# Kernel optimization log

Measured on AMD Instinct MI355X. Metric: run time of the kernel, lower is better.

Reference implementation:

```python
import jax, jax.numpy as jnp
import numpy as np

A_CUBIC = -0.5  # Keys cubic-convolution parameter (order-3 spline approximation)


def _cubic(t):
    # Keys cubic interpolation kernel, support (-2, 2)
    at = jnp.abs(t)
    at2 = at * at
    at3 = at2 * at
    a = A_CUBIC
    w_inner = (a + 2.0) * at3 - (a + 3.0) * at2 + 1.0          # |t| <= 1
    w_outer = a * at3 - 5.0 * a * at2 + 8.0 * a * at - 4.0 * a  # 1 < |t| < 2
    return jnp.where(at <= 1.0, w_inner, jnp.where(at < 2.0, w_outer, 0.0))


def _spline_upsample_matrix(n_out, n_ctrl):
    # (n_out, n_ctrl) dense weight matrix interpolating control points to the
    # full-resolution axis with the cubic kernel; edge taps clamped (nearest).
    u = jnp.arange(n_out, dtype=jnp.float32) * (n_ctrl - 1) / (n_out - 1)
    i0 = jnp.floor(u).astype(jnp.int32)
    taps = i0[:, None] + jnp.arange(-1, 3)                      # (n_out, 4)
    w = _cubic(u[:, None] - taps.astype(jnp.float32))           # (n_out, 4)
    taps_c = jnp.clip(taps, 0, n_ctrl - 1)
    B = jnp.zeros((n_out, n_ctrl), jnp.float32)
    B = B.at[jnp.arange(n_out)[:, None], taps_c].add(w)
    return B


def _elastic_warp(img, displacement):
    # img: (H, W, C); displacement: (2, 3, 3) control-point displacements (dy, dx)
    H, W, C = img.shape
    By = _spline_upsample_matrix(H, displacement.shape[1])      # (H, 3)
    Bx = _spline_upsample_matrix(W, displacement.shape[2])      # (W, 3)
    disp = jnp.einsum('hy,dyx,wx->dhw', By, displacement, Bx)   # (2, H, W)

    yy = jnp.arange(H, dtype=jnp.float32)[:, None] + disp[0]    # sample coords
    xx = jnp.arange(W, dtype=jnp.float32)[None, :] + disp[1]
    iy0 = jnp.floor(yy).astype(jnp.int32)
    ix0 = jnp.floor(xx).astype(jnp.int32)

    out = jnp.zeros_like(img)
    # 4x4 cubic tap stencil (fixed small loop; each iteration is one full gather)
    for a in range(-1, 3):
        ty = iy0 + a
        wy = _cubic(yy - ty.astype(jnp.float32))                # (H, W)
        tyc = jnp.clip(ty, 0, H - 1)
        for b in range(-1, 3):
            tx = ix0 + b
            wx = _cubic(xx - tx.astype(jnp.float32))            # (H, W)
            txc = jnp.clip(tx, 0, W - 1)
            out = out + (wy * wx)[..., None] * img[tyc, txc]    # gather (H,W,C)
    return out


def setup_inputs() -> dict:
    key = jax.random.key(0)
    k1, k2 = jax.random.split(key)
    H, W, C = 2048, 4096, 3
    inputs = jax.random.normal(k1, (H, W, C), dtype=jnp.float32)
    displacement = jax.random.normal(k2, (2, 3, 3), dtype=jnp.float32)
    return {"inputs": inputs, "displacement": displacement}


def reference(inputs, displacement):
    # module draws displacement ~ N(0,1)*5 internally; externalized here
    return _elastic_warp(inputs, displacement * 5.0)
```

## Files before the change

kernel.cpp:

```cpp
#include <hip/hip_runtime.h>
#include <math.h>

constexpr int H = 2048;
constexpr int W = 4096;
constexpr int RS = W * 3;

__device__ __forceinline__ float k_inner(float t) {
    return fmaf(fmaf(1.5f, t, -2.5f), t * t, 1.0f);
}
__device__ __forceinline__ float k_outer(float t) {
    return fmaf(fmaf(fmaf(-0.5f, t, 2.5f), t, -4.0f), t, 2.0f);
}
__device__ __forceinline__ float cubic_w(float t) {
    float at = fabsf(t);
    if (at <= 1.0f) return k_inner(at);
    if (at < 2.0f)  return k_outer(at);
    return 0.0f;
}

__global__ __launch_bounds__(256)
void elastic_warp_kernel(const float* __restrict__ img,
                         const float* __restrict__ dctrl,
                         float* __restrict__ out) {
    int x0 = blockIdx.x << 4;
    int y0 = blockIdx.y << 4;

    int t = threadIdx.x;
    int lane = t & 63;
    int wave = t >> 6;
    int xi = lane & 15;
    int gi = lane >> 4;
    int r  = (wave << 2) + gi;

    int h = y0 + r;
    int w = x0 + xi;

    __shared__ float s_cy[16][6];
    if (t < 16) {
        int hh = y0 + t;
        float u = (float)(2 * hh) / (float)(H - 1);
        float i0 = floorf(u);
        float by0 = 0.f, by1 = 0.f, by2 = 0.f;
#pragma unroll
        for (int k = -1; k < 3; ++k) {
            float tap = i0 + (float)k;
            float wt = cubic_w(u - tap);
            int tc = (int)tap;
            tc = tc < 0 ? 0 : (tc > 2 ? 2 : tc);
            if (tc == 0) by0 += wt; else if (tc == 1) by1 += wt; else by2 += wt;
        }
#pragma unroll
        for (int x = 0; x < 3; ++x) {
            s_cy[t][x]     = 5.0f * (by0 * dctrl[x]     + by1 * dctrl[3 + x]  + by2 * dctrl[6 + x]);
            s_cy[t][3 + x] = 5.0f * (by0 * dctrl[9 + x] + by1 * dctrl[12 + x] + by2 * dctrl[15 + x]);
        }
    }
    __syncthreads();

    float cy0 = s_cy[r][0], cy1 = s_cy[r][1], cy2 = s_cy[r][2];
    float cy3 = s_cy[r][3], cy4 = s_cy[r][4], cy5 = s_cy[r][5];

    float u = (float)w * (2.0f / 4095.0f);
    bool hiu = u >= 1.0f;
    float s = u - (hiu ? 1.0f : 0.0f);
    float o1 = k_outer(1.0f + s);
    float is = k_inner(s);
    float i1 = k_inner(1.0f - s);
    float o2 = k_outer(2.0f - s);
    float bx0 = hiu ? o1 : (o1 + is);
    float bx1 = hiu ? is : i1;
    float bx2 = hiu ? (i1 + o2) : o2;

    float d0 = cy0 * bx0 + cy1 * bx1 + cy2 * bx2;
    float d1 = cy3 * bx0 + cy4 * bx1 + cy5 * bx2;

    float yy = (float)h + d0;
    float xx = (float)w + d1;
    float iy0f = floorf(yy);
    float ix0f = floorf(xx);
    float fy = yy - iy0f;
    float fx = xx - ix0f;
    int iy0 = (int)iy0f;
    int ix0 = (int)ix0f;

    float wy0 = k_outer(1.0f + fy), wy1 = k_inner(fy), wy2 = k_inner(1.0f - fy), wy3 = k_outer(2.0f - fy);
    float wx0 = k_outer(1.0f + fx), wx1 = k_inner(fx), wx2 = k_inner(1.0f - fx), wx3 = k_outer(2.0f - fx);

    float acc0 = 0.0f, acc1 = 0.0f, acc2 = 0.0f;

    bool interior = (iy0 >= 1) & (iy0 <= H - 3) & (ix0 >= 1) & (ix0 <= W - 3);
    if (interior) {
        int off = ((iy0 - 1) * W + (ix0 - 1)) * 3;
        const float* b0 = img + off;
        const float* b1 = b0 + RS;
        const float* b2 = b1 + RS;
        const float* b3 = b2 + RS;

        float4 v00 = ((const float4*)b0)[0];
        float4 v01 = ((const float4*)b0)[1];
        float4 v02 = ((const float4*)b0)[2];
        float4 v10 = ((const float4*)b1)[0];
        float4 v11 = ((const float4*)b1)[1];
        float4 v12 = ((const float4*)b1)[2];
        float4 v20 = ((const float4*)b2)[0];
        float4 v21 = ((const float4*)b2)[1];
        float4 v22 = ((const float4*)b2)[2];
        float4 v30 = ((const float4*)b3)[0];
        float4 v31 = ((const float4*)b3)[1];
        float4 v32 = ((const float4*)b3)[2];

        float q0, q1, q2, q3;
        q0 = wy0 * wx0; q1 = wy0 * wx1; q2 = wy0 * wx2; q3 = wy0 * wx3;
        acc0 = fmaf(q0, v00.x, fmaf(q1, v00.w, fmaf(q2, v01.z, fmaf(q3, v02.y, acc0))));
        acc1 = fmaf(q0, v00.y, fmaf(q1, v01.x, fmaf(q2, v01.w, fmaf(q3, v02.z, acc1))));
        acc2 = fmaf(q0, v00.z, fmaf(q1, v01.y, fmaf(q2, v02.x, fmaf(q3, v02.w, acc2))));

        q0 = wy1 * wx0; q1 = wy1 * wx1; q2 = wy1 * wx2; q3 = wy1 * wx3;
        acc0 = fmaf(q0, v10.x, fmaf(q1, v10.w, fmaf(q2, v11.z, fmaf(q3, v12.y, acc0))));
        acc1 = fmaf(q0, v10.y, fmaf(q1, v11.x, fmaf(q2, v11.w, fmaf(q3, v12.z, acc1))));
        acc2 = fmaf(q0, v10.z, fmaf(q1, v11.y, fmaf(q2, v12.x, fmaf(q3, v12.w, acc2))));

        q0 = wy2 * wx0; q1 = wy2 * wx1; q2 = wy2 * wx2; q3 = wy2 * wx3;
        acc0 = fmaf(q0, v20.x, fmaf(q1, v20.w, fmaf(q2, v21.z, fmaf(q3, v22.y, acc0))));
        acc1 = fmaf(q0, v20.y, fmaf(q1, v21.x, fmaf(q2, v21.w, fmaf(q3, v22.z, acc1))));
        acc2 = fmaf(q0, v20.z, fmaf(q1, v21.y, fmaf(q2, v22.x, fmaf(q3, v22.w, acc2))));

        q0 = wy3 * wx0; q1 = wy3 * wx1; q2 = wy3 * wx2; q3 = wy3 * wx3;
        acc0 = fmaf(q0, v30.x, fmaf(q1, v30.w, fmaf(q2, v31.z, fmaf(q3, v32.y, acc0))));
        acc1 = fmaf(q0, v30.y, fmaf(q1, v31.x, fmaf(q2, v31.w, fmaf(q3, v32.z, acc1))));
        acc2 = fmaf(q0, v30.z, fmaf(q1, v31.y, fmaf(q2, v32.x, fmaf(q3, v32.w, acc2))));
    } else {
        float wy[4] = {wy0, wy1, wy2, wy3};
        float wx[4] = {wx0, wx1, wx2, wx3};
#pragma unroll
        for (int a = 0; a < 4; ++a) {
            int ty = iy0 + a - 1;
            ty = ty < 0 ? 0 : (ty > H - 1 ? H - 1 : ty);
            int rowoff = ty * RS;
            float ay = wy[a];
#pragma unroll
            for (int b = 0; b < 4; ++b) {
                int tx = ix0 + b - 1;
                tx = tx < 0 ? 0 : (tx > W - 1 ? W - 1 : tx);
                float wgt = ay * wx[b];
                const float* p = img + rowoff + tx * 3;
                acc0 += wgt * p[0];
                acc1 += wgt * p[1];
                acc2 += wgt * p[2];
            }
        }
    }

    int oo = (h * W + w) * 3;
    out[oo + 0] = acc0;
    out[oo + 1] = acc1;
    out[oo + 2] = acc2;
}

extern "C" void kernel_launch(void* const* d_in, const int* in_sizes, int n_in,
                              void* d_out, int out_size, void* d_ws, size_t ws_size,
                              hipStream_t stream) {
    const float* img   = (const float*)d_in[0];
    const float* dctrl = (const float*)d_in[1];
    float* out = (float*)d_out;

    dim3 grid(W / 16, H / 16);
    elastic_warp_kernel<<<grid, 256, 0, stream>>>(img, dctrl, out);
}
```

Baseline: 64.55 us.

## Process four 16-wide column strips per thread, factor separable stencil, nontemporal stores

Each block now covers 64 columns by 16 rows, with every thread looping over four pixels. This amortizes the per-block shared-memory setup of the y spline coefficients and the barrier, and cuts the grid to a quarter of its previous size. The 4x4 stencil is evaluated separably: x weights are applied per row, then y weights combine the four rows, which needs fewer multiplies. Output writes use nontemporal stores so they do not pollute the cache, at the cost of fewer waves for latency hiding and more registers per thread.

```diff
diff --git a/kernel.cpp b/kernel.cpp
--- a/kernel.cpp
+++ b/kernel.cpp
@@ -22,8 +22,8 @@
 void elastic_warp_kernel(const float* __restrict__ img,
                          const float* __restrict__ dctrl,
                          float* __restrict__ out) {
-    int x0 = blockIdx.x << 4;
-    int y0 = blockIdx.y << 4;
+    int x0r = blockIdx.x << 6;
+    int y0  = blockIdx.y << 4;
 
     int t = threadIdx.x;
     int lane = t & 63;
@@ -31,9 +31,6 @@
     int xi = lane & 15;
     int gi = lane >> 4;
     int r  = (wave << 2) + gi;
-
-    int h = y0 + r;
-    int w = x0 + xi;
 
     __shared__ float s_cy[16][6];
     if (t < 16) {
@@ -57,104 +54,112 @@
     }
     __syncthreads();
 
+    int h = y0 + r;
+    float hf = (float)h;
     float cy0 = s_cy[r][0], cy1 = s_cy[r][1], cy2 = s_cy[r][2];
     float cy3 = s_cy[r][3], cy4 = s_cy[r][4], cy5 = s_cy[r][5];
+    int rowbase = h * W;
 
-    float u = (float)w * (2.0f / 4095.0f);
-    bool hiu = u >= 1.0f;
-    float s = u - (hiu ? 1.0f : 0.0f);
-    float o1 = k_outer(1.0f + s);
-    float is = k_inner(s);
-    float i1 = k_inner(1.0f - s);
-    float o2 = k_outer(2.0f - s);
-    float bx0 = hiu ? o1 : (o1 + is);
-    float bx1 = hiu ? is : i1;
-    float bx2 = hiu ? (i1 + o2) : o2;
+#pragma unroll
+    for (int it = 0; it < 4; ++it) {
+        int w = x0r + (it << 4) + xi;
 
-    float d0 = cy0 * bx0 + cy1 * bx1 + cy2 * bx2;
-    float d1 = cy3 * bx0 + cy4 * bx1 + cy5 * bx2;
+        float u = (float)w * (2.0f / 4095.0f);
+        bool hiu = u >= 1.0f;
+        float s = u - (hiu ? 1.0f : 0.0f);
+        float o1 = k_outer(1.0f + s);
+        float is = k_inner(s);
+        float i1 = k_inner(1.0f - s);
+        float o2 = k_outer(2.0f - s);
+        float bx0 = hiu ? o1 : (o1 + is);
+        float bx1 = hiu ? is : i1;
+        float bx2 = hiu ? (i1 + o2) : o2;
 
-    float yy = (float)h + d0;
-    float xx = (float)w + d1;
-    float iy0f = floorf(yy);
-    float ix0f = floorf(xx);
-    float fy = yy - iy0f;
-    float fx = xx - ix0f;
-    int iy0 = (int)iy0f;
-    int ix0 = (int)ix0f;
+        float d0 = cy0 * bx0 + cy1 * bx1 + cy2 * bx2;
+        float d1 = cy3 * bx0 + cy4 * bx1 + cy5 * bx2;
 
-    float wy0 = k_outer(1.0f + fy), wy1 = k_inner(fy), wy2 = k_inner(1.0f - fy), wy3 = k_outer(2.0f - fy);
-    float wx0 = k_outer(1.0f + fx), wx1 = k_inner(fx), wx2 = k_inner(1.0f - fx), wx3 = k_outer(2.0f - fx);
+        float yy = hf + d0;
+        float xx = (float)w + d1;
+        float iy0f = floorf(yy);
+        float ix0f = floorf(xx);
+        float fy = yy - iy0f;
+        float fx = xx - ix0f;
+        int iy0 = (int)iy0f;
+        int ix0 = (int)ix0f;
 
-    float acc0 = 0.0f, acc1 = 0.0f, acc2 = 0.0f;
+        float wy0 = k_outer(1.0f + fy), wy1 = k_inner(fy), wy2 = k_inner(1.0f - fy), wy3 = k_outer(2.0f - fy);
+        float wx0 = k_outer(1.0f + fx), wx1 = k_inner(fx), wx2 = k_inner(1.0f - fx), wx3 = k_outer(2.0f - fx);
 
-    bool interior = (iy0 >= 1) & (iy0 <= H - 3) & (ix0 >= 1) & (ix0 <= W - 3);
-    if (interior) {
-        int off = ((iy0 - 1) * W + (ix0 - 1)) * 3;
-        const float* b0 = img + off;
-        const float* b1 = b0 + RS;
-        const float* b2 = b1 + RS;
-        const float* b3 = b2 + RS;
+        float acc0, acc1, acc2;
 
-        float4 v00 = ((const float4*)b0)[0];
-        float4 v01 = ((const float4*)b0)[1];
-        float4 v02 = ((const float4*)b0)[2];
-        float4 v10 = ((const float4*)b1)[0];
-        float4 v11 = ((const float4*)b1)[1];
-        float4 v12 = ((const float4*)b1)[2];
-        float4 v20 = ((const float4*)b2)[0];
-        float4 v21 = ((const float4*)b2)[1];
-        float4 v22 = ((const float4*)b2)[2];
-        float4 v30 = ((const float4*)b3)[0];
-        float4 v31 = ((const float4*)b3)[1];
-        float4 v32 = ((const float4*)b3)[2];
+        bool interior = (iy0 >= 1) & (iy0 <= H - 3) & (ix0 >= 1) & (ix0 <= W - 3);
+        if (interior) {
+            int off = ((iy0 - 1) * W + (ix0 - 1)) * 3;
+            const float* b0 = img + off;
+            const float* b1 = b0 + RS;
+            const float* b2 = b1 + RS;
+            const float* b3 = b2 + RS;
 
-        float q0, q1, q2, q3;
-        q0 = wy0 * wx0; q1 = wy0 * wx1; q2 = wy0 * wx2; q3 = wy0 * wx3;
-        acc0 = fmaf(q0, v00.x, fmaf(q1, v00.w, fmaf(q2, v01.z, fmaf(q3, v02.y, acc0))));
-        acc1 = fmaf(q0, v00.y, fmaf(q1, v01.x, fmaf(q2, v01.w, fmaf(q3, v02.z, acc1))));
-        acc2 = fmaf(q0, v00.z, fmaf(q1, v01.y, fmaf(q2, v02.x, fmaf(q3, v02.w, acc2))));
+            float4 v00 = ((const float4*)b0)[0];
+            float4 v01 = ((const float4*)b0)[1];
+            float4 v02 = ((const float4*)b0)[2];
+            float4 v10 = ((const float4*)b1)[0];
+            float4 v11 = ((const float4*)b1)[1];
+            float4 v12 = ((const float4*)b1)[2];
+            float4 v20 = ((const float4*)b2)[0];
+            float4 v21 = ((const float4*)b2)[1];
+            float4 v22 = ((const float4*)b2)[2];
+            float4 v30 = ((const float4*)b3)[0];
+            float4 v31 = ((const float4*)b3)[1];
+            float4 v32 = ((const float4*)b3)[2];
 
-        q0 = wy1 * wx0; q1 = wy1 * wx1; q2 = wy1 * wx2; q3 = wy1 * wx3;
-        acc0 = fmaf(q0, v10.x, fmaf(q1, v10.w, fmaf(q2, v11.z, fmaf(q3, v12.y, acc0))));
-        acc1 = fmaf(q0, v10.y, fmaf(q1, v11.x, fmaf(q2, v11.w, fmaf(q3, v12.z, acc1))));
-        acc2 = fmaf(q0, v10.z, fmaf(q1, v11.y, fmaf(q2, v12.x, fmaf(q3, v12.w, acc2))));
+            float t00 = fmaf(wx0, v00.x, fmaf(wx1, v00.w, fmaf(wx2, v01.z, wx3 * v02.y)));
+            float t01 = fmaf(wx0, v00.y, fmaf(wx1, v01.x, fmaf(wx2, v01.w, wx3 * v02.z)));
+            float t02 = fmaf(wx0, v00.z, fmaf(wx1, v01.y, fmaf(wx2, v02.x, wx3 * v02.w)));
 
-        q0 = wy2 * wx0; q1 = wy2 * wx1; q2 = wy2 * wx2; q3 = wy2 * wx3;
-        acc0 = fmaf(q0, v20.x, fmaf(q1, v20.w, fmaf(q2, v21.z, fmaf(q3, v22.y, acc0))));
-        acc1 = fmaf(q0, v20.y, fmaf(q1, v21.x, fmaf(q2, v21.w, fmaf(q3, v22.z, acc1))));
-        acc2 = fmaf(q0, v20.z, fmaf(q1, v21.y, fmaf(q2, v22.x, fmaf(q3, v22.w, acc2))));
+            float t10 = fmaf(wx0, v10.x, fmaf(wx1, v10.w, fmaf(wx2, v11.z, wx3 * v12.y)));
+            float t11 = fmaf(wx0, v10.y, fmaf(wx1, v11.x, fmaf(wx2, v11.w, wx3 * v12.z)));
+            float t12 = fmaf(wx0, v10.z, fmaf(wx1, v11.y, fmaf(wx2, v12.x, wx3 * v12.w)));
 
-        q0 = wy3 * wx0; q1 = wy3 * wx1; q2 = wy3 * wx2; q3 = wy3 * wx3;
-        acc0 = fmaf(q0, v30.x, fmaf(q1, v30.w, fmaf(q2, v31.z, fmaf(q3, v32.y, acc0))));
-        acc1 = fmaf(q0, v30.y, fmaf(q1, v31.x, fmaf(q2, v31.w, fmaf(q3, v32.z, acc1))));
-        acc2 = fmaf(q0, v30.z, fmaf(q1, v31.y, fmaf(q2, v32.x, fmaf(q3, v32.w, acc2))));
-    } else {
-        float wy[4] = {wy0, wy1, wy2, wy3};
-        float wx[4] = {wx0, wx1, wx2, wx3};
+            float t20 = fmaf(wx0, v20.x, fmaf(wx1, v20.w, fmaf(wx2, v21.z, wx3 * v22.y)));
+            float t21 = fmaf(wx0, v20.y, fmaf(wx1, v21.x, fmaf(wx2, v21.w, wx3 * v22.z)));
+            float t22 = fmaf(wx0, v20.z, fmaf(wx1, v21.y, fmaf(wx2, v22.x, wx3 * v22.w)));
+
+            float t30 = fmaf(wx0, v30.x, fmaf(wx1, v30.w, fmaf(wx2, v31.z, wx3 * v32.y)));
+            float t31 = fmaf(wx0, v30.y, fmaf(wx1, v31.x, fmaf(wx2, v31.w, wx3 * v32.z)));
+            float t32 = fmaf(wx0, v30.z, fmaf(wx1, v31.y, fmaf(wx2, v32.x, wx3 * v32.w)));
+
+            acc0 = fmaf(wy0, t00, fmaf(wy1, t10, fmaf(wy2, t20, wy3 * t30)));
+            acc1 = fmaf(wy0, t01, fmaf(wy1, t11, fmaf(wy2, t21, wy3 * t31)));
+            acc2 = fmaf(wy0, t02, fmaf(wy1, t12, fmaf(wy2, t22, wy3 * t32)));
+        } else {
+            acc0 = 0.f; acc1 = 0.f; acc2 = 0.f;
+            float wy[4] = {wy0, wy1, wy2, wy3};
+            float wx[4] = {wx0, wx1, wx2, wx3};
 #pragma unroll
-        for (int a = 0; a < 4; ++a) {
-            int ty = iy0 + a - 1;
-            ty = ty < 0 ? 0 : (ty > H - 1 ? H - 1 : ty);
-            int rowoff = ty * RS;
-            float ay = wy[a];
+            for (int a = 0; a < 4; ++a) {
+                int ty = iy0 + a - 1;
+                ty = ty < 0 ? 0 : (ty > H - 1 ? H - 1 : ty);
+                int rowoff = ty * RS;
+                float ay = wy[a];
 #pragma unroll
-            for (int b = 0; b < 4; ++b) {
-                int tx = ix0 + b - 1;
-                tx = tx < 0 ? 0 : (tx > W - 1 ? W - 1 : tx);
-                float wgt = ay * wx[b];
-                const float* p = img + rowoff + tx * 3;
-                acc0 += wgt * p[0];
-                acc1 += wgt * p[1];
-                acc2 += wgt * p[2];
+                for (int b = 0; b < 4; ++b) {
+                    int tx = ix0 + b - 1;
+                    tx = tx < 0 ? 0 : (tx > W - 1 ? W - 1 : tx);
+                    float wgt = ay * wx[b];
+                    const float* p = img + rowoff + tx * 3;
+                    acc0 += wgt * p[0];
+                    acc1 += wgt * p[1];
+                    acc2 += wgt * p[2];
+                }
             }
         }
+
+        int oo = (rowbase + w) * 3;
+        __builtin_nontemporal_store(acc0, out + oo);
+        __builtin_nontemporal_store(acc1, out + oo + 1);
+        __builtin_nontemporal_store(acc2, out + oo + 2);
     }
-
-    int oo = (h * W + w) * 3;
-    out[oo + 0] = acc0;
-    out[oo + 1] = acc1;
-    out[oo + 2] = acc2;
 }
 
 extern "C" void kernel_launch(void* const* d_in, const int* in_sizes, int n_in,
@@ -164,6 +169,6 @@
     const float* dctrl = (const float*)d_in[1];
     float* out = (float*)d_out;
 
-    dim3 grid(W / 16, H / 16);
+    dim3 grid(W / 64, H / 16);
     elastic_warp_kernel<<<grid, 256, 0, stream>>>(img, dctrl, out);
 }
```

Result: faster. 62.17 us (-3.7%).
